# Performance work log

Measured on AMD Instinct MI355X. Metric: run time of the kernel, lower is better.

Reference implementation:

```python
import jax, jax.numpy as jnp
import numpy as np

N_NODES = 50000
N_EDGES = 600000
DIM = 128
N_HEADS = 3
EDGE_VOCAB = 22754
NEG_SLOPE = 0.2


def setup_inputs() -> dict:
    key = jax.random.key(0)
    ks = jax.random.split(key, 12)
    s = 1.0 / np.sqrt(DIM)
    return {
        "x": jax.random.normal(ks[0], (N_NODES, DIM), dtype=jnp.float32),
        "edge_index": jax.random.randint(ks[1], (2, N_EDGES), 0, N_NODES, dtype=jnp.int64),
        "edge_ids": jax.random.randint(ks[2], (N_EDGES,), 0, EDGE_VOCAB, dtype=jnp.int64),
        "ddi_weight": jax.random.uniform(ks[3], (N_EDGES,), dtype=jnp.float32),
        "W_lin": jax.random.normal(ks[4], (DIM, DIM), dtype=jnp.float32) * s,
        "b_lin": jnp.zeros((DIM,), dtype=jnp.float32),
        "edge_emb": jax.random.normal(ks[5], (EDGE_VOCAB, 1), dtype=jnp.float32) * 0.1,
        "W_heads": jax.random.normal(ks[6], (N_HEADS, DIM, DIM), dtype=jnp.float32) * s,
        "att_src": jax.random.normal(ks[7], (N_HEADS, DIM), dtype=jnp.float32) * s,
        "att_dst": jax.random.normal(ks[8], (N_HEADS, DIM), dtype=jnp.float32) * s,
        "bias_heads": jnp.zeros((N_HEADS, DIM), dtype=jnp.float32),
    }


def _gat_head(x, src, dst, ew, W, a_src, a_dst, bias):
    # x: [N, D] (already passed through shared lin), ew: [E] scalar edge weights
    h = x @ W                                   # [N, D]
    e = jax.nn.leaky_relu(
        (h @ a_src)[src] + (h @ a_dst)[dst], NEG_SLOPE)   # [E]
    # segment softmax over destination nodes
    e_max = jax.ops.segment_max(e, dst, num_segments=N_NODES)   # [N]
    e_exp = jnp.exp(e - e_max[dst])                              # [E]
    denom = jax.ops.segment_sum(e_exp, dst, num_segments=N_NODES)
    alpha = e_exp / jnp.maximum(denom[dst], 1e-16)               # [E]
    msg = (alpha * ew)[:, None] * h[src]                         # [E, D]
    return jax.ops.segment_sum(msg, dst, num_segments=N_NODES) + bias


def reference(x, edge_index, edge_ids, ddi_weight, W_lin, b_lin, edge_emb,
              W_heads, att_src, att_dst, bias_heads):
    x = x @ W_lin + b_lin                         # shared linear projection
    ew = edge_emb[edge_ids, 0] - ddi_weight        # [E]
    src, dst = edge_index[0], edge_index[1]
    out = jnp.zeros_like(x)
    for hix in range(N_HEADS):                     # small fixed head count
        out = out + _gat_head(x, src, dst, ew, W_heads[hix],
                              att_src[hix], att_dst[hix], bias_heads[hix])
    return out / N_HEADS
```

## Files before the change

### kernel.cpp

```cpp
#include <hip/hip_runtime.h>
#include <math.h>

#define NN 50000
#define NE 600000
#define D 128
#define NH 3
#define CAP 64
#define EDGE_BLOCKS ((NE + 255) / 256)
#define MFMA_BLOCKS ((NN + 63) / 64)
#define LOG2E 1.44269504088896340736f

typedef short bf16x8 __attribute__((ext_vector_type(8)));
typedef _Float16 f16x8 __attribute__((ext_vector_type(8)));
typedef float f32x4 __attribute__((ext_vector_type(4)));

__device__ __forceinline__ unsigned short f2b(float f) {
  unsigned int u = __float_as_uint(f);
  u += 0x7FFF + ((u >> 16) & 1);
  return (unsigned short)(u >> 16);
}
__device__ __forceinline__ float blo(unsigned int u) {
  return __uint_as_float(u << 16);
}
__device__ __forceinline__ float bhi(unsigned int u) {
  return __uint_as_float(u & 0xffff0000u);
}
__device__ __forceinline__ unsigned short f2h(float f) {
  _Float16 t = (_Float16)f;
  return *(unsigned short*)&t;
}

__global__ __launch_bounds__(256) void pack_scatter2(const float* __restrict__ W_lin,
                                                     const float* __restrict__ W_heads,
                                                     const float* __restrict__ att_src,
                                                     const float* __restrict__ att_dst,
                                                     const float* __restrict__ b_lin,
                                                     const float* __restrict__ bias_heads,
                                                     const int* __restrict__ ei,
                                                     const int* __restrict__ eid,
                                                     const float* __restrict__ ddi,
                                                     const float* __restrict__ emb,
                                                     uint4* __restrict__ Bpack,
                                                     uint4* __restrict__ Wpack3,
                                                     float* __restrict__ sbuf,
                                                     float* __restrict__ bcomb2,
                                                     int* __restrict__ counts,
                                                     unsigned int* __restrict__ slots8) {
  const int bx = blockIdx.x;
  const int tid = threadIdx.x;
  if (bx < EDGE_BLOCKS) {
    int e = bx * 256 + tid;
    if (e < NE) {
      int src = ei[e], dst = ei[NE + e];
      int idx = atomicAdd(&counts[dst], 1);
      idx = idx < CAP ? idx : CAP - 1;
      float ew = emb[eid[e]] - ddi[e];
      slots8[dst * CAP + idx] = (unsigned int)src | ((unsigned int)f2b(ew) << 16);
    }
    return;
  }
  const int pb = bx - EDGE_BLOCKS;
  if (pb < 8) {
    int r = pb * 256 + tid;
    int nt = r >> 8, s = (r >> 6) & 3, q = (r >> 4) & 3, n0 = r & 15;
    int kbase = s * 32 + q * 8;
    int n = nt * 16 + n0;
    unsigned int w[4];
    #pragma unroll
    for (int p = 0; p < 4; ++p) {
      unsigned short lo = f2b(W_lin[(kbase + 2 * p) * D + n]);
      unsigned short hi = f2b(W_lin[(kbase + 2 * p + 1) * D + n]);
      w[p] = (unsigned int)lo | ((unsigned int)hi << 16);
    }
    Bpack[r] = make_uint4(w[0], w[1], w[2], w[3]);
  } else if (pb < 32) {
    int u = (pb - 8) * 256 + tid;
    int h = u >> 11, r = u & 2047;
    int nt = r >> 8, s = (r >> 6) & 3, q = (r >> 4) & 3, n0 = r & 15;
    int kbase = s * 32 + q * 8;
    int n = nt * 16 + n0;
    const float* W = W_heads + (size_t)h * D * D;
    unsigned int w[4];
    #pragma unroll
    for (int p = 0; p < 4; ++p) {
      unsigned short lo = f2h(W[(kbase + 2 * p) * D + n]);
      unsigned short hi = f2h(W[(kbase + 2 * p + 1) * D + n]);
      w[p] = (unsigned int)lo | ((unsigned int)hi << 16);
    }
    Wpack3[h * 2048 + r] = make_uint4(w[0], w[1], w[2], w[3]);
  } else if (pb < 35) {
    const int h = pb - 32;
    __shared__ float wha_s[128], wha_d[128], scs[128], scd[128];
    {
      int m = tid & 127;
      const float* W = W_heads + (size_t)h * D * D + m * D;
      const float* a = (tid < 128) ? (att_src + h * D) : (att_dst + h * D);
      float acc = 0.f;
      for (int n = 0; n < D; ++n) acc += W[n] * a[n];
      if (tid < 128) wha_s[m] = acc; else wha_d[m] = acc;
    }
    __syncthreads();
    {
      int k = tid & 127;
      const float* wl = W_lin + k * D;
      const float* wha = (tid < 128) ? wha_s : wha_d;
      float acc = 0.f;
      for (int m = 0; m < D; ++m) acc += wl[m] * wha[m];
      if (tid < 128) scs[k] = acc * LOG2E; else scd[k] = acc * LOG2E;
    }
    __syncthreads();
    if (tid < 2) {
      const float* wha = tid ? wha_d : wha_s;
      float a = 0.f;
      for (int k = 0; k < D; ++k) a += b_lin[k] * wha[k];
      sbuf[h * 2 + tid] = a * LOG2E;
    }
    {
      int s = (tid >> 6) & 3, q = (tid >> 4) & 3, n0 = tid & 15;
      int kbase = s * 32 + q * 8;
      bool mine = (n0 < 6) && ((n0 >> 1) == h);
      bool zero = (h == 0) && (n0 >= 6);
      if (mine || zero) {
        float vals[8];
        #pragma unroll
        for (int j = 0; j < 8; ++j)
          vals[j] = zero ? 0.f : ((n0 & 1) ? scd[kbase + j] : scs[kbase + j]);
        unsigned int w[4];
        #pragma unroll
        for (int p = 0; p < 4; ++p)
          w[p] = (unsigned int)f2b(vals[2 * p]) | ((unsigned int)f2b(vals[2 * p + 1]) << 16);
        Bpack[2048 + tid] = make_uint4(w[0], w[1], w[2], w[3]);
      }
    }
  } else {
    if (tid < D)
      bcomb2[tid] = (bias_heads[tid] + bias_heads[D + tid] + bias_heads[2 * D + tid]) * (1.f / 3.f);
  }
}

__global__ __launch_bounds__(256) void mfma_x(const float* __restrict__ x,
                                              const uint4* __restrict__ Bpack,
                                              const float* __restrict__ b_lin,
                                              const float* __restrict__ sbuf,
                                              unsigned short* __restrict__ xb,
                                              float* __restrict__ s_src4,
                                              float* __restrict__ s_dst4) {
  const int row0 = blockIdx.x * 64;
  const int tid = threadIdx.x;
  __shared__ __align__(16) unsigned short As[64][136];
  #pragma unroll
  for (int it = 0; it < 8; ++it) {
    int idx = tid + it * 256;
    int m = idx >> 5, k4 = idx & 31;
    int row = row0 + m;
    float4 v = make_float4(0.f, 0.f, 0.f, 0.f);
    if (row < NN) v = ((const float4*)(x + (size_t)row * D))[k4];
    uint2 pk;
    pk.x = (unsigned int)f2b(v.x) | ((unsigned int)f2b(v.y) << 16);
    pk.y = (unsigned int)f2b(v.z) | ((unsigned int)f2b(v.w) << 16);
    *((uint2*)&As[m][k4 * 4]) = pk;
  }
  __syncthreads();
  const int wv = tid >> 6;
  const int lane = tid & 63;
  const int n0 = lane & 15, q = lane >> 4;
  const int boff = q * 16 + n0;
  const bf16x8* Bp = (const bf16x8*)Bpack;

  bf16x8 a4[4];
  #pragma unroll
  for (int s = 0; s < 4; ++s)
    a4[s] = *(const bf16x8*)&As[wv * 16 + n0][s * 32 + q * 8];

  f32x4 acc[9];
  #pragma unroll
  for (int nt = 0; nt < 9; ++nt) acc[nt] = (f32x4){0.f, 0.f, 0.f, 0.f};

  #pragma unroll
  for (int s = 0; s < 4; ++s) {
    #pragma unroll
    for (int nt = 0; nt < 9; ++nt) {
      bf16x8 b = Bp[(nt * 4 + s) * 64 + boff];
      acc[nt] = __builtin_amdgcn_mfma_f32_16x16x32_bf16(a4[s], b, acc[nt], 0, 0, 0);
    }
  }
  __syncthreads();
  #pragma unroll
  for (int nt = 0; nt < 8; ++nt) {
    int col = nt * 16 + n0;
    float bv = b_lin[col];
    #pragma unroll
    for (int r = 0; r < 4; ++r)
      As[wv * 16 + q * 4 + r][col] = f2b(acc[nt][r] + bv);
  }
  if (n0 < 6) {
    float sb = sbuf[n0];
    float* Sout = (n0 & 1) ? s_dst4 : s_src4;
    #pragma unroll
    for (int r = 0; r < 4; ++r) {
      int row = row0 + wv * 16 + q * 4 + r;
      if (row < NN) Sout[row * 4 + (n0 >> 1)] = acc[8][r] + sb;
    }
  }
  __syncthreads();
  #pragma unroll
  for (int i = 0; i < 4; ++i) {
    int idx = tid + i * 256;
    int row = idx >> 4, c16 = idx & 15;
    int grow = row0 + row;
    if (grow < NN)
      *((uint4*)&xb[(size_t)grow * D + c16 * 8]) = *((const uint4*)&As[row][c16 * 8]);
  }
}

__global__ __launch_bounds__(64) void gather12(const int* __restrict__ counts,
                                               const unsigned int* __restrict__ slots8,
                                               const float4* __restrict__ s_src4,
                                               const float4* __restrict__ s_dst4,
                                               const unsigned short* __restrict__ xb,
                                               unsigned short* __restrict__ accb) {
  const int dst = blockIdx.x;
  const int lane = threadIdx.x;
  const int hf = lane >> 5;
  const int c = (lane & 31) * 4;
  int cnt = counts[dst];
  cnt = cnt < CAP ? cnt : CAP;
  const int beg = dst * CAP;
  const int end = beg + cnt;
  float4 sd = s_dst4[dst];
  float a0[4] = {0.f, 0.f, 0.f, 0.f};
  float a1[4] = {0.f, 0.f, 0.f, 0.f};
  float a2[4] = {0.f, 0.f, 0.f, 0.f};
  float d0 = 0.f, d1 = 0.f, d2 = 0.f;
  int s = beg + hf;
  for (; s + 2 < end; s += 4) {
    unsigned int seA = slots8[s];
    unsigned int seB = slots8[s + 2];
    int srcA = seA & 0xffffu, srcB = seB & 0xffffu;
    float ewA = bhi(seA), ewB = bhi(seB);
    float4 ssA = s_src4[srcA];
    float4 ssB = s_src4[srcB];
    uint2 ua = *(const uint2*)&xb[(size_t)srcA * D + c];
    uint2 ub = *(const uint2*)&xb[(size_t)srcB * D + c];
    float vA0 = ssA.x + sd.x, vA1 = ssA.y + sd.y, vA2 = ssA.z + sd.z;
    float vB0 = ssB.x + sd.x, vB1 = ssB.y + sd.y, vB2 = ssB.z + sd.z;
    vA0 = vA0 > 0.f ? vA0 : 0.2f * vA0;
    vA1 = vA1 > 0.f ? vA1 : 0.2f * vA1;
    vA2 = vA2 > 0.f ? vA2 : 0.2f * vA2;
    vB0 = vB0 > 0.f ? vB0 : 0.2f * vB0;
    vB1 = vB1 > 0.f ? vB1 : 0.2f * vB1;
    vB2 = vB2 > 0.f ? vB2 : 0.2f * vB2;
    float pA0 = exp2f(vA0), pA1 = exp2f(vA1), pA2 = exp2f(vA2);
    float pB0 = exp2f(vB0), pB1 = exp2f(vB1), pB2 = exp2f(vB2);
    float wa0 = pA0 * ewA, wa1 = pA1 * ewA, wa2 = pA2 * ewA;
    float wb0 = pB0 * ewB, wb1 = pB1 * ewB, wb2 = pB2 * ewB;
    float xA[4] = {blo(ua.x), bhi(ua.x), blo(ua.y), bhi(ua.y)};
    float xB[4] = {blo(ub.x), bhi(ub.x), blo(ub.y), bhi(ub.y)};
    #pragma unroll
    for (int j = 0; j < 4; ++j) {
      a0[j] += wa0 * xA[j] + wb0 * xB[j];
      a1[j] += wa1 * xA[j] + wb1 * xB[j];
      a2[j] += wa2 * xA[j] + wb2 * xB[j];
    }
    d0 += pA0 + pB0;
    d1 += pA1 + pB1;
    d2 += pA2 + pB2;
  }
  if (s < end) {
    unsigned int seA = slots8[s];
    int srcA = seA & 0xffffu;
    float ewA = bhi(seA);
    float4 ssA = s_src4[srcA];
    uint2 ua = *(const uint2*)&xb[(size_t)srcA * D + c];
    float vA0 = ssA.x + sd.x, vA1 = ssA.y + sd.y, vA2 = ssA.z + sd.z;
    vA0 = vA0 > 0.f ? vA0 : 0.2f * vA0;
    vA1 = vA1 > 0.f ? vA1 : 0.2f * vA1;
    vA2 = vA2 > 0.f ? vA2 : 0.2f * vA2;
    float pA0 = exp2f(vA0), pA1 = exp2f(vA1), pA2 = exp2f(vA2);
    float w0 = pA0 * ewA, w1 = pA1 * ewA, w2 = pA2 * ewA;
    float xA[4] = {blo(ua.x), bhi(ua.x), blo(ua.y), bhi(ua.y)};
    #pragma unroll
    for (int j = 0; j < 4; ++j) {
      a0[j] += w0 * xA[j];
      a1[j] += w1 * xA[j];
      a2[j] += w2 * xA[j];
    }
    d0 += pA0; d1 += pA1; d2 += pA2;
  }
  #pragma unroll
  for (int j = 0; j < 4; ++j) {
    a0[j] += __shfl_xor(a0[j], 32, 64);
    a1[j] += __shfl_xor(a1[j], 32, 64);
    a2[j] += __shfl_xor(a2[j], 32, 64);
  }
  d0 += __shfl_xor(d0, 32, 64);
  d1 += __shfl_xor(d1, 32, 64);
  d2 += __shfl_xor(d2, 32, 64);
  if (hf == 0) {
    float r0 = 1.f / (3.f * fmaxf(d0, 1e-16f));
    float r1 = 1.f / (3.f * fmaxf(d1, 1e-16f));
    float r2 = 1.f / (3.f * fmaxf(d2, 1e-16f));
    unsigned short* base = accb + (size_t)dst * (NH * D);
    uint2 o;
    o.x = (unsigned int)f2h(a0[0] * r0) | ((unsigned int)f2h(a0[1] * r0) << 16);
    o.y = (unsigned int)f2h(a0[2] * r0) | ((unsigned int)f2h(a0[3] * r0) << 16);
    *(uint2*)&base[c] = o;
    o.x = (unsigned int)f2h(a1[0] * r1) | ((unsigned int)f2h(a1[1] * r1) << 16);
    o.y = (unsigned int)f2h(a1[2] * r1) | ((unsigned int)f2h(a1[3] * r1) << 16);
    *(uint2*)&base[D + c] = o;
    o.x = (unsigned int)f2h(a2[0] * r2) | ((unsigned int)f2h(a2[1] * r2) << 16);
    o.y = (unsigned int)f2h(a2[2] * r2) | ((unsigned int)f2h(a2[3] * r2) << 16);
    *(uint2*)&base[2 * D + c] = o;
  }
}

__global__ __launch_bounds__(256) void final_gemm16(const unsigned short* __restrict__ accb,
                                                    const uint4* __restrict__ Wpack3,
                                                    const float* __restrict__ bcomb2,
                                                    float* __restrict__ out) {
  const int row0 = blockIdx.x * 64;
  const int tid = threadIdx.x;
  __shared__ __align__(16) _Float16 Af[64][136];
  const int wv = tid >> 6;
  const int lane = tid & 63;
  const int n0 = lane & 15, q = lane >> 4;
  const int boff = q * 16 + n0;

  f32x4 o[8];
  #pragma unroll
  for (int nt = 0; nt < 8; ++nt) o[nt] = (f32x4){0.f, 0.f, 0.f, 0.f};

  for (int ck = 0; ck < NH; ++ck) {
    if (ck) __syncthreads();
    #pragma unroll
    for (int it = 0; it < 4; ++it) {
      int idx = tid + it * 256;
      int m = idx >> 4, k8 = idx & 15;
      int row = row0 + m;
      uint4 u = make_uint4(0, 0, 0, 0);
      if (row < NN)
        u = *(const uint4*)&accb[(size_t)row * (NH * D) + ck * D + k8 * 8];
      *((uint4*)&Af[m][k8 * 8]) = u;
    }
    __syncthreads();
    f16x8 af[4];
    #pragma unroll
    for (int s = 0; s < 4; ++s)
      af[s] = *(const f16x8*)&Af[wv * 16 + n0][s * 32 + q * 8];
    const f16x8* Bp = (const f16x8*)(Wpack3 + ck * 2048);
    #pragma unroll
    for (int s = 0; s < 4; ++s) {
      #pragma unroll
      for (int nt = 0; nt < 8; ++nt) {
        f16x8 b = Bp[(nt * 4 + s) * 64 + boff];
        o[nt] = __builtin_amdgcn_mfma_f32_16x16x32_f16(af[s], b, o[nt], 0, 0, 0);
      }
    }
  }
  #pragma unroll
  for (int nt = 0; nt < 8; ++nt) {
    int col = nt * 16 + n0;
    float bv = bcomb2[col];
    #pragma unroll
    for (int r = 0; r < 4; ++r) {
      int row = row0 + wv * 16 + q * 4 + r;
      if (row < NN) out[(size_t)row * D + col] = o[nt][r] + bv;
    }
  }
}

extern "C" void kernel_launch(void* const* d_in, const int* in_sizes, int n_in,
                              void* d_out, int out_size, void* d_ws, size_t ws_size,
                              hipStream_t stream) {
  const float* x          = (const float*)d_in[0];
  const int*   ei         = (const int*)d_in[1];
  const int*   eid        = (const int*)d_in[2];
  const float* ddi        = (const float*)d_in[3];
  const float* W_lin      = (const float*)d_in[4];
  const float* b_lin      = (const float*)d_in[5];
  const float* emb        = (const float*)d_in[6];
  const float* W_heads    = (const float*)d_in[7];
  const float* att_src    = (const float*)d_in[8];
  const float* att_dst    = (const float*)d_in[9];
  const float* bias_heads = (const float*)d_in[10];
  float* out = (float*)d_out;

  uint4*  Bpack  = (uint4*)d_ws;
  uint4*  Wpack3 = Bpack + 2304;
  unsigned short* xb = (unsigned short*)(Wpack3 + NH * 2048);
  unsigned int* slots8 = (unsigned int*)(xb + (size_t)NN * D);
  unsigned short* accb = (unsigned short*)(slots8 + (size_t)NN * CAP);
  float*  sbuf   = (float*)(accb + (size_t)NN * NH * D);
  float*  bcomb2 = sbuf + 8;
  float*  s_src4 = bcomb2 + 128;
  float*  s_dst4 = s_src4 + (size_t)NN * 4;
  int*    counts = (int*)(s_dst4 + (size_t)NN * 4);

  hipMemsetAsync(counts, 0, (size_t)NN * sizeof(int), stream);
  pack_scatter2<<<EDGE_BLOCKS + 36, 256, 0, stream>>>(
      W_lin, W_heads, att_src, att_dst, b_lin, bias_heads, ei, eid, ddi, emb,
      Bpack, Wpack3, sbuf, bcomb2, counts, slots8);
  mfma_x<<<MFMA_BLOCKS, 256, 0, stream>>>(x, Bpack, b_lin, sbuf, xb,
                                          s_src4, s_dst4);
  gather12<<<NN, 64, 0, stream>>>(counts, slots8, (const float4*)s_src4,
                                  (const float4*)s_dst4, xb, accb);
  final_gemm16<<<MFMA_BLOCKS, 256, 0, stream>>>(accb, Wpack3, bcomb2, out);
}
```

Baseline: 215.5 us.

## Fuse edge scatter with node projection and compute attention scores in separate blocks

```diff
diff --git a/kernel.cpp b/kernel.cpp
--- a/kernel.cpp
+++ b/kernel.cpp
@@ -6,8 +6,10 @@
 #define D 128
 #define NH 3
 #define CAP 64
-#define EDGE_BLOCKS ((NE + 255) / 256)
-#define MFMA_BLOCKS ((NN + 63) / 64)
+#define SCAT_BLOCKS ((NE + 127) / 128)
+#define MF_BLOCKS ((NN + 31) / 32)
+#define SC_BLOCKS ((NN + 255) / 256)
+#define FG_BLOCKS ((NN + 63) / 64)
 #define LOG2E 1.44269504088896340736f
 
 typedef short bf16x8 __attribute__((ext_vector_type(8)));
@@ -30,26 +32,73 @@
   return *(unsigned short*)&t;
 }
 
-__global__ __launch_bounds__(256) void pack_scatter2(const float* __restrict__ W_lin,
-                                                     const float* __restrict__ W_heads,
-                                                     const float* __restrict__ att_src,
-                                                     const float* __restrict__ att_dst,
-                                                     const float* __restrict__ b_lin,
-                                                     const float* __restrict__ bias_heads,
-                                                     const int* __restrict__ ei,
-                                                     const int* __restrict__ eid,
-                                                     const float* __restrict__ ddi,
-                                                     const float* __restrict__ emb,
-                                                     uint4* __restrict__ Bpack,
-                                                     uint4* __restrict__ Wpack3,
-                                                     float* __restrict__ sbuf,
-                                                     float* __restrict__ bcomb2,
-                                                     int* __restrict__ counts,
-                                                     unsigned int* __restrict__ slots8) {
+__global__ __launch_bounds__(256) void prep0(const float* __restrict__ W_lin,
+                                             const float* __restrict__ W_heads,
+                                             const float* __restrict__ bias_heads,
+                                             uint4* __restrict__ Bpack,
+                                             uint4* __restrict__ Wpack3,
+                                             float* __restrict__ bcomb2,
+                                             int* __restrict__ counts) {
   const int bx = blockIdx.x;
   const int tid = threadIdx.x;
-  if (bx < EDGE_BLOCKS) {
-    int e = bx * 256 + tid;
+  if (bx < 49) {
+    int i = bx * 256 + tid;
+    if (i < NN / 4) ((int4*)counts)[i] = make_int4(0, 0, 0, 0);
+  } else if (bx < 57) {
+    int r = (bx - 49) * 256 + tid;
+    int nt = r >> 8, s = (r >> 6) & 3, q = (r >> 4) & 3, n0 = r & 15;
+    int kbase = s * 32 + q * 8;
+    int n = nt * 16 + n0;
+    unsigned int w[4];
+    #pragma unroll
+    for (int p = 0; p < 4; ++p) {
+      unsigned short lo = f2b(W_lin[(kbase + 2 * p) * D + n]);
+      unsigned short hi = f2b(W_lin[(kbase + 2 * p + 1) * D + n]);
+      w[p] = (unsigned int)lo | ((unsigned int)hi << 16);
+    }
+    Bpack[r] = make_uint4(w[0], w[1], w[2], w[3]);
+  } else if (bx < 81) {
+    int u = (bx - 57) * 256 + tid;
+    int h = u >> 11, r = u & 2047;
+    int nt = r >> 8, s = (r >> 6) & 3, q = (r >> 4) & 3, n0 = r & 15;
+    int kbase = s * 32 + q * 8;
+    int n = nt * 16 + n0;
+    const float* W = W_heads + (size_t)h * D * D;
+    unsigned int w[4];
+    #pragma unroll
+    for (int p = 0; p < 4; ++p) {
+      unsigned short lo = f2h(W[(kbase + 2 * p) * D + n]);
+      unsigned short hi = f2h(W[(kbase + 2 * p + 1) * D + n]);
+      w[p] = (unsigned int)lo | ((unsigned int)hi << 16);
+    }
+    Wpack3[h * 2048 + r] = make_uint4(w[0], w[1], w[2], w[3]);
+  } else {
+    if (tid < D)
+      bcomb2[tid] = (bias_heads[tid] + bias_heads[D + tid] + bias_heads[2 * D + tid]) * (1.f / 3.f);
+  }
+}
+
+__global__ __launch_bounds__(128) void scatmm(const float* __restrict__ x,
+                                              const uint4* __restrict__ Bpack,
+                                              const float* __restrict__ b_lin,
+                                              const float* __restrict__ W_lin,
+                                              const float* __restrict__ W_heads,
+                                              const float* __restrict__ att_src,
+                                              const float* __restrict__ att_dst,
+                                              const int* __restrict__ ei,
+                                              const int* __restrict__ eid,
+                                              const float* __restrict__ ddi,
+                                              const float* __restrict__ emb,
+                                              unsigned short* __restrict__ xb,
+                                              float* __restrict__ s_src4,
+                                              float* __restrict__ s_dst4,
+                                              int* __restrict__ counts,
+                                              unsigned int* __restrict__ slots8) {
+  const int bx = blockIdx.x;
+  const int tid = threadIdx.x;
+  __shared__ __align__(16) unsigned char smem[8704];
+  if (bx < SCAT_BLOCKS) {
+    int e = bx * 128 + tid;
     if (e < NE) {
       int src = ei[e], dst = ei[NE + e];
       int idx = atomicAdd(&counts[dst], 1);
@@ -57,159 +106,114 @@
       float ew = emb[eid[e]] - ddi[e];
       slots8[dst * CAP + idx] = (unsigned int)src | ((unsigned int)f2b(ew) << 16);
     }
-    return;
-  }
-  const int pb = bx - EDGE_BLOCKS;
-  if (pb < 8) {
-    int r = pb * 256 + tid;
-    int nt = r >> 8, s = (r >> 6) & 3, q = (r >> 4) & 3, n0 = r & 15;
-    int kbase = s * 32 + q * 8;
-    int n = nt * 16 + n0;
-    unsigned int w[4];
-    #pragma unroll
-    for (int p = 0; p < 4; ++p) {
-      unsigned short lo = f2b(W_lin[(kbase + 2 * p) * D + n]);
-      unsigned short hi = f2b(W_lin[(kbase + 2 * p + 1) * D + n]);
-      w[p] = (unsigned int)lo | ((unsigned int)hi << 16);
-    }
-    Bpack[r] = make_uint4(w[0], w[1], w[2], w[3]);
-  } else if (pb < 32) {
-    int u = (pb - 8) * 256 + tid;
-    int h = u >> 11, r = u & 2047;
-    int nt = r >> 8, s = (r >> 6) & 3, q = (r >> 4) & 3, n0 = r & 15;
-    int kbase = s * 32 + q * 8;
-    int n = nt * 16 + n0;
-    const float* W = W_heads + (size_t)h * D * D;
-    unsigned int w[4];
-    #pragma unroll
-    for (int p = 0; p < 4; ++p) {
-      unsigned short lo = f2h(W[(kbase + 2 * p) * D + n]);
-      unsigned short hi = f2h(W[(kbase + 2 * p + 1) * D + n]);
-      w[p] = (unsigned int)lo | ((unsigned int)hi << 16);
-    }
-    Wpack3[h * 2048 + r] = make_uint4(w[0], w[1], w[2], w[3]);
-  } else if (pb < 35) {
-    const int h = pb - 32;
-    __shared__ float wha_s[128], wha_d[128], scs[128], scd[128];
+  } else if (bx < SCAT_BLOCKS + MF_BLOCKS) {
+    unsigned short (*As)[136] = (unsigned short(*)[136])smem;
+    const int row0 = (bx - SCAT_BLOCKS) * 32;
+    #pragma unroll
+    for (int it = 0; it < 8; ++it) {
+      int idx = tid + it * 128;
+      int m = idx >> 5, k4 = idx & 31;
+      int row = row0 + m;
+      float4 v = make_float4(0.f, 0.f, 0.f, 0.f);
+      if (row < NN) v = ((const float4*)(x + (size_t)row * D))[k4];
+      uint2 pk;
+      pk.x = (unsigned int)f2b(v.x) | ((unsigned int)f2b(v.y) << 16);
+      pk.y = (unsigned int)f2b(v.z) | ((unsigned int)f2b(v.w) << 16);
+      *((uint2*)&As[m][k4 * 4]) = pk;
+    }
+    __syncthreads();
+    const int wv = tid >> 6;
+    const int lane = tid & 63;
+    const int n0 = lane & 15, q = lane >> 4;
+    const int boff = q * 16 + n0;
+    const bf16x8* Bp = (const bf16x8*)Bpack;
+    bf16x8 a4[4];
+    #pragma unroll
+    for (int s = 0; s < 4; ++s)
+      a4[s] = *(const bf16x8*)&As[wv * 16 + n0][s * 32 + q * 8];
+    f32x4 acc[8];
+    #pragma unroll
+    for (int nt = 0; nt < 8; ++nt) acc[nt] = (f32x4){0.f, 0.f, 0.f, 0.f};
+    #pragma unroll
+    for (int s = 0; s < 4; ++s) {
+      #pragma unroll
+      for (int nt = 0; nt < 8; ++nt) {
+        bf16x8 b = Bp[(nt * 4 + s) * 64 + boff];
+        acc[nt] = __builtin_amdgcn_mfma_f32_16x16x32_bf16(a4[s], b, acc[nt], 0, 0, 0);
+      }
+    }
+    __syncthreads();
+    #pragma unroll
+    for (int nt = 0; nt < 8; ++nt) {
+      int col = nt * 16 + n0;
+      float bv = b_lin[col];
+      #pragma unroll
+      for (int r = 0; r < 4; ++r)
+        As[wv * 16 + q * 4 + r][col] = f2b(acc[nt][r] + bv);
+    }
+    __syncthreads();
+    #pragma unroll
+    for (int i = 0; i < 4; ++i) {
+      int idx = tid + i * 128;
+      int row = idx >> 4, c16 = idx & 15;
+      int grow = row0 + row;
+      if (grow < NN)
+        *((uint4*)&xb[(size_t)grow * D + c16 * 8]) = *((const uint4*)&As[row][c16 * 8]);
+    }
+  } else {
+    float* wha = (float*)smem;
+    float* scs = wha + 128 * 8;
+    scs = wha + 1024;
+    __shared__ float sbv[8];
+    const int row0 = (bx - (SCAT_BLOCKS + MF_BLOCKS)) * 256;
+    const int t = tid;
+    #pragma unroll
+    for (int h = 0; h < NH; ++h) {
+      const float* Wr = W_heads + (size_t)h * D * D + t * D;
+      const float* as = att_src + h * D;
+      const float* ad = att_dst + h * D;
+      float aS = 0.f, aD = 0.f;
+      for (int n = 0; n < D; ++n) { float w = Wr[n]; aS += w * as[n]; aD += w * ad[n]; }
+      wha[t * 8 + 2 * h] = aS;
+      wha[t * 8 + 2 * h + 1] = aD;
+    }
+    __syncthreads();
     {
-      int m = tid & 127;
-      const float* W = W_heads + (size_t)h * D * D + m * D;
-      const float* a = (tid < 128) ? (att_src + h * D) : (att_dst + h * D);
-      float acc = 0.f;
-      for (int n = 0; n < D; ++n) acc += W[n] * a[n];
-      if (tid < 128) wha_s[m] = acc; else wha_d[m] = acc;
-    }
-    __syncthreads();
-    {
-      int k = tid & 127;
-      const float* wl = W_lin + k * D;
-      const float* wha = (tid < 128) ? wha_s : wha_d;
-      float acc = 0.f;
-      for (int m = 0; m < D; ++m) acc += wl[m] * wha[m];
-      if (tid < 128) scs[k] = acc * LOG2E; else scd[k] = acc * LOG2E;
-    }
-    __syncthreads();
-    if (tid < 2) {
-      const float* wha = tid ? wha_d : wha_s;
+      const float* wl = W_lin + t * D;
+      float a[6] = {0.f, 0.f, 0.f, 0.f, 0.f, 0.f};
+      for (int m = 0; m < D; ++m) {
+        float w = wl[m];
+        #pragma unroll
+        for (int j = 0; j < 6; ++j) a[j] += w * wha[m * 8 + j];
+      }
+      #pragma unroll
+      for (int j = 0; j < 6; ++j) scs[t * 8 + j] = a[j] * LOG2E;
+    }
+    if (t < 6) {
       float a = 0.f;
-      for (int k = 0; k < D; ++k) a += b_lin[k] * wha[k];
-      sbuf[h * 2 + tid] = a * LOG2E;
-    }
-    {
-      int s = (tid >> 6) & 3, q = (tid >> 4) & 3, n0 = tid & 15;
-      int kbase = s * 32 + q * 8;
-      bool mine = (n0 < 6) && ((n0 >> 1) == h);
-      bool zero = (h == 0) && (n0 >= 6);
-      if (mine || zero) {
-        float vals[8];
+      for (int k = 0; k < D; ++k) a += b_lin[k] * wha[k * 8 + t];
+      sbv[t] = a * LOG2E;
+    }
+    __syncthreads();
+    for (int rr = 0; rr < 2; ++rr) {
+      int row = row0 + rr * 128 + t;
+      if (row < NN) {
+        const float4* xr = (const float4*)(x + (size_t)row * D);
+        float a[6] = {0.f, 0.f, 0.f, 0.f, 0.f, 0.f};
+        for (int k4 = 0; k4 < 32; ++k4) {
+          float4 v = xr[k4];
+          const float* s0 = &scs[(k4 * 4) * 8];
+          #pragma unroll
+          for (int j = 0; j < 6; ++j)
+            a[j] += v.x * s0[j] + v.y * s0[8 + j] + v.z * s0[16 + j] + v.w * s0[24 + j];
+        }
         #pragma unroll
-        for (int j = 0; j < 8; ++j)
-          vals[j] = zero ? 0.f : ((n0 & 1) ? scd[kbase + j] : scs[kbase + j]);
-        unsigned int w[4];
-        #pragma unroll
-        for (int p = 0; p < 4; ++p)
-          w[p] = (unsigned int)f2b(vals[2 * p]) | ((unsigned int)f2b(vals[2 * p + 1]) << 16);
-        Bpack[2048 + tid] = make_uint4(w[0], w[1], w[2], w[3]);
+        for (int h = 0; h < NH; ++h) {
+          s_src4[row * 4 + h] = a[2 * h] + sbv[2 * h];
+          s_dst4[row * 4 + h] = a[2 * h + 1] + sbv[2 * h + 1];
+        }
       }
     }
-  } else {
-    if (tid < D)
-      bcomb2[tid] = (bias_heads[tid] + bias_heads[D + tid] + bias_heads[2 * D + tid]) * (1.f / 3.f);
-  }
-}
-
-__global__ __launch_bounds__(256) void mfma_x(const float* __restrict__ x,
-                                              const uint4* __restrict__ Bpack,
-                                              const float* __restrict__ b_lin,
-                                              const float* __restrict__ sbuf,
-                                              unsigned short* __restrict__ xb,
-                                              float* __restrict__ s_src4,
-                                              float* __restrict__ s_dst4) {
-  const int row0 = blockIdx.x * 64;
-  const int tid = threadIdx.x;
-  __shared__ __align__(16) unsigned short As[64][136];
-  #pragma unroll
-  for (int it = 0; it < 8; ++it) {
-    int idx = tid + it * 256;
-    int m = idx >> 5, k4 = idx & 31;
-    int row = row0 + m;
-    float4 v = make_float4(0.f, 0.f, 0.f, 0.f);
-    if (row < NN) v = ((const float4*)(x + (size_t)row * D))[k4];
-    uint2 pk;
-    pk.x = (unsigned int)f2b(v.x) | ((unsigned int)f2b(v.y) << 16);
-    pk.y = (unsigned int)f2b(v.z) | ((unsigned int)f2b(v.w) << 16);
-    *((uint2*)&As[m][k4 * 4]) = pk;
-  }
-  __syncthreads();
-  const int wv = tid >> 6;
-  const int lane = tid & 63;
-  const int n0 = lane & 15, q = lane >> 4;
-  const int boff = q * 16 + n0;
-  const bf16x8* Bp = (const bf16x8*)Bpack;
-
-  bf16x8 a4[4];
-  #pragma unroll
-  for (int s = 0; s < 4; ++s)
-    a4[s] = *(const bf16x8*)&As[wv * 16 + n0][s * 32 + q * 8];
-
-  f32x4 acc[9];
-  #pragma unroll
-  for (int nt = 0; nt < 9; ++nt) acc[nt] = (f32x4){0.f, 0.f, 0.f, 0.f};
-
-  #pragma unroll
-  for (int s = 0; s < 4; ++s) {
-    #pragma unroll
-    for (int nt = 0; nt < 9; ++nt) {
-      bf16x8 b = Bp[(nt * 4 + s) * 64 + boff];
-      acc[nt] = __builtin_amdgcn_mfma_f32_16x16x32_bf16(a4[s], b, acc[nt], 0, 0, 0);
-    }
-  }
-  __syncthreads();
-  #pragma unroll
-  for (int nt = 0; nt < 8; ++nt) {
-    int col = nt * 16 + n0;
-    float bv = b_lin[col];
-    #pragma unroll
-    for (int r = 0; r < 4; ++r)
-      As[wv * 16 + q * 4 + r][col] = f2b(acc[nt][r] + bv);
-  }
-  if (n0 < 6) {
-    float sb = sbuf[n0];
-    float* Sout = (n0 & 1) ? s_dst4 : s_src4;
-    #pragma unroll
-    for (int r = 0; r < 4; ++r) {
-      int row = row0 + wv * 16 + q * 4 + r;
-      if (row < NN) Sout[row * 4 + (n0 >> 1)] = acc[8][r] + sb;
-    }
-  }
-  __syncthreads();
-  #pragma unroll
-  for (int i = 0; i < 4; ++i) {
-    int idx = tid + i * 256;
-    int row = idx >> 4, c16 = idx & 15;
-    int grow = row0 + row;
-    if (grow < NN)
-      *((uint4*)&xb[(size_t)grow * D + c16 * 8]) = *((const uint4*)&As[row][c16 * 8]);
   }
 }
 
@@ -390,19 +394,17 @@
   unsigned short* xb = (unsigned short*)(Wpack3 + NH * 2048);
   unsigned int* slots8 = (unsigned int*)(xb + (size_t)NN * D);
   unsigned short* accb = (unsigned short*)(slots8 + (size_t)NN * CAP);
-  float*  sbuf   = (float*)(accb + (size_t)NN * NH * D);
-  float*  bcomb2 = sbuf + 8;
+  float*  bcomb2 = (float*)(accb + (size_t)NN * NH * D);
   float*  s_src4 = bcomb2 + 128;
   float*  s_dst4 = s_src4 + (size_t)NN * 4;
   int*    counts = (int*)(s_dst4 + (size_t)NN * 4);
 
-  hipMemsetAsync(counts, 0, (size_t)NN * sizeof(int), stream);
-  pack_scatter2<<<EDGE_BLOCKS + 36, 256, 0, stream>>>(
-      W_lin, W_heads, att_src, att_dst, b_lin, bias_heads, ei, eid, ddi, emb,
-      Bpack, Wpack3, sbuf, bcomb2, counts, slots8);
-  mfma_x<<<MFMA_BLOCKS, 256, 0, stream>>>(x, Bpack, b_lin, sbuf, xb,
-                                          s_src4, s_dst4);
+  prep0<<<82, 256, 0, stream>>>(W_lin, W_heads, bias_heads, Bpack, Wpack3,
+                                bcomb2, counts);
+  scatmm<<<SCAT_BLOCKS + MF_BLOCKS + SC_BLOCKS, 128, 0, stream>>>(
+      x, Bpack, b_lin, W_lin, W_heads, att_src, att_dst, ei, eid, ddi, emb,
+      xb, s_src4, s_dst4, counts, slots8);
   gather12<<<NN, 64, 0, stream>>>(counts, slots8, (const float4*)s_src4,
                                   (const float4*)s_dst4, xb, accb);
-  final_gemm16<<<MFMA_BLOCKS, 256, 0, stream>>>(accb, Wpack3, bcomb2, out);
-}
+  final_gemm16<<<FG_BLOCKS, 256, 0, stream>>>(accb, Wpack3, bcomb2, out);
+}
```

Result: slower. 249.2 us (+15.6%).
